# Kernel optimization log

Hardware: AMD Instinct MI355X
Metric: run time of the kernel (lower is better)

Reference implementation:

```python
import jax, jax.numpy as jnp
import numpy as np
from jax import lax

N_QUANTIZE = 256
N_AUX = 28
N_RESCH = 512
N_SKIPCH = 256
KS = 2
DILATIONS = [2 ** i for i in range(10)] * 3  # 30 layers
L = len(DILATIONS)


def _causal_conv(x, w, b, d):
    # x: (B, Cin, T), w: (Cout, Cin, KS) torch Conv1d layout, left-pad => causal
    pad = (w.shape[-1] - 1) * d
    y = lax.conv_general_dilated(x, w, window_strides=(1,), padding=[(pad, 0)],
                                 rhs_dilation=(d,),
                                 dimension_numbers=('NCH', 'OIH', 'NCH'))
    return y + b[None, :, None]


def _conv1x1(x, w, b):
    # x: (B, Cin, T), w: (Cout, Cin)
    return jnp.einsum('oi,bit->bot', w, x) + b[None, :, None]


def setup_inputs() -> dict:
    key = jax.random.key(0)
    ks = jax.random.split(key, 20)
    B, T = 2, 8000
    s = 0.05
    rn = lambda k, shape: (jax.random.normal(k, shape, jnp.float32) * s)
    inp = {
        'x': jax.random.randint(ks[0], (B, T), 0, N_QUANTIZE),
        'h': jax.random.normal(ks[1], (B, N_AUX, T), jnp.float32),
        'causal_w': rn(ks[2], (N_RESCH, N_QUANTIZE, KS)),
        'causal_b': rn(ks[3], (N_RESCH,)),
        'dil_sig_w': rn(ks[4], (L, N_RESCH, N_RESCH, KS)),
        'dil_sig_b': rn(ks[5], (L, N_RESCH)),
        'dil_tanh_w': rn(ks[6], (L, N_RESCH, N_RESCH, KS)),
        'dil_tanh_b': rn(ks[7], (L, N_RESCH)),
        'aux_sig_w': rn(ks[8], (L, N_RESCH, N_AUX)),
        'aux_sig_b': rn(ks[9], (L, N_RESCH)),
        'aux_tanh_w': rn(ks[10], (L, N_RESCH, N_AUX)),
        'aux_tanh_b': rn(ks[11], (L, N_RESCH)),
        'skip_w': rn(ks[12], (L, N_SKIPCH, N_RESCH)),
        'skip_b': rn(ks[13], (L, N_SKIPCH)),
        'res_w': rn(ks[14], (L, N_RESCH, N_RESCH)),
        'res_b': rn(ks[15], (L, N_RESCH)),
        'post1_w': rn(ks[16], (N_SKIPCH, N_SKIPCH)),
        'post1_b': rn(ks[17], (N_SKIPCH,)),
        'post2_w': rn(ks[18], (N_QUANTIZE, N_SKIPCH)),
        'post2_b': rn(ks[19], (N_QUANTIZE,)),
    }
    return inp


def reference(x, h, causal_w, causal_b, dil_sig_w, dil_sig_b, dil_tanh_w, dil_tanh_b,
              aux_sig_w, aux_sig_b, aux_tanh_w, aux_tanh_b, skip_w, skip_b,
              res_w, res_b, post1_w, post1_b, post2_w, post2_b):
    B, T = x.shape
    # _preprocess: onehot (B,T,Q) -> (B,Q,T), then causal conv
    oh = jax.nn.one_hot(x % N_QUANTIZE, N_QUANTIZE, dtype=jnp.float32).transpose(0, 2, 1)
    out = _causal_conv(oh, causal_w, causal_b, 1)  # (B, n_resch, T)
    skip_sum = jnp.zeros((B, N_SKIPCH, T), jnp.float32)
    for l, d in enumerate(DILATIONS):
        sig = _causal_conv(out, dil_sig_w[l], dil_sig_b[l], d) + _conv1x1(h, aux_sig_w[l], aux_sig_b[l])
        tan = _causal_conv(out, dil_tanh_w[l], dil_tanh_b[l], d) + _conv1x1(h, aux_tanh_w[l], aux_tanh_b[l])
        z = jax.nn.sigmoid(sig) * jnp.tanh(tan)
        skip_sum = skip_sum + _conv1x1(z, skip_w[l], skip_b[l])
        out = _conv1x1(z, res_w[l], res_b[l]) + out
    # _postprocess: relu -> 1x1 -> relu -> 1x1 -> (B, T, n_quantize)
    y = jax.nn.relu(skip_sum)
    y = jax.nn.relu(_conv1x1(y, post1_w, post1_b))
    y = _conv1x1(y, post2_w, post2_b)
    return y.transpose(0, 2, 1)
```

## Files before the change

### kernel.cpp

```cpp
#include <hip/hip_runtime.h>
#include <math.h>

#define T_LEN 8000
#define BATCH 2
#define CCH 512
#define SKP 256
#define AUXP 32
#define NQ 256
#define NLAYER 30
#define PADF 512
#define TPAD 8192
#define ROWS (PADF + TPAD)
#define HROWS TPAD

typedef unsigned short hfu;
typedef unsigned int u32;
typedef __attribute__((ext_vector_type(8))) _Float16 half8;
typedef __attribute__((ext_vector_type(4))) float f32x4;

#define GLOAD16(g, l)                                                          \
  __builtin_amdgcn_global_load_lds(                                            \
      (const __attribute__((address_space(1))) void*)(g),                      \
      (__attribute__((address_space(3))) void*)(l), 16, 0, 0)

__device__ inline hfu hfbits(float f) {
  union { _Float16 h; hfu u; } x;
  x.h = (_Float16)f;
  return x.u;
}
__device__ inline u32 pk2(float a, float b) {
  return (u32)hfbits(a) | ((u32)hfbits(b) << 16);
}
__device__ inline uint4 pk8(const float f[8]) {
  return make_uint4(pk2(f[0], f[1]), pk2(f[2], f[3]), pk2(f[4], f[5]), pk2(f[6], f[7]));
}
__device__ inline int ldsL(int row, int ck) {
  return ((row >> 1) << 3) + ((((ck) ^ ((row >> 1) & 3)) << 1) | (row & 1));
}

__global__ __launch_bounds__(256) void zero16(uint4* p, int n) {
  for (int i = blockIdx.x * 256 + threadIdx.x; i < n; i += gridDim.x * 256)
    p[i] = make_uint4(0u, 0u, 0u, 0u);
}

__global__ __launch_bounds__(256) void cvt_dil2(const float* __restrict__ inS,
                                                const float* __restrict__ inT,
                                                hfu* __restrict__ outS, hfu* __restrict__ outT) {
  const long NG = (long)NLAYER * CCH * (CCH / 4);
  for (long g2 = (long)blockIdx.x * 256 + threadIdx.x; g2 < 2 * NG; g2 += (long)gridDim.x * 256) {
    const int sel = (int)(g2 >= NG);
    const long g = sel ? (g2 - NG) : g2;
    const float* in = sel ? inT : inS;
    hfu* out = sel ? outT : outS;
    const int i4 = (int)(g & 127) * 4;
    const int o = (int)((g >> 7) & 511);
    const int l = (int)(g >> 16);
    const float* pp = in + (((size_t)l * CCH + o) * CCH + i4) * 2;
    float4 f0 = *(const float4*)pp;
    float4 f1 = *(const float4*)(pp + 4);
    uint2 t0 = make_uint2(pk2(f0.x, f0.z), pk2(f1.x, f1.z));
    uint2 t1 = make_uint2(pk2(f0.y, f0.w), pk2(f1.y, f1.w));
    hfu* ob = out + ((size_t)l * 2 * CCH + o) * CCH + i4;
    *(uint2*)ob = t0;
    *(uint2*)(ob + (size_t)CCH * CCH) = t1;
  }
}

__global__ __launch_bounds__(256) void cvt_skipres(const float* __restrict__ skw,
                                                   const float* __restrict__ rsw,
                                                   hfu* __restrict__ out) {
  const long NG = (long)NLAYER * 768 * (CCH / 4);
  for (long g = (long)blockIdx.x * 256 + threadIdx.x; g < NG; g += (long)gridDim.x * 256) {
    const int i4 = (int)(g & 127) * 4;
    const int r = (int)((g >> 7) % 768);
    const int l = (int)(g / (128 * 768));
    const float* src = (r < SKP) ? (skw + ((size_t)l * SKP + r) * CCH + i4)
                                 : (rsw + ((size_t)l * CCH + (r - SKP)) * CCH + i4);
    float4 f = *(const float4*)src;
    *(uint2*)(out + ((size_t)l * 768 + r) * CCH + i4) = make_uint2(pk2(f.x, f.y), pk2(f.z, f.w));
  }
}

__global__ __launch_bounds__(256) void cvt_aux(const float* __restrict__ in, hfu* __restrict__ out) {
  const int N = NLAYER * CCH * AUXP;
  for (int i = blockIdx.x * 256 + threadIdx.x; i < N; i += gridDim.x * 256) {
    const int j = i & 31;
    const int o = (i >> 5) & 511;
    const int l = i >> 14;
    float v = (j < 28) ? in[((size_t)l * CCH + o) * 28 + j] : 0.f;
    out[i] = hfbits(v);
  }
}

__global__ __launch_bounds__(256) void cvt_copy(const float* __restrict__ in, hfu* __restrict__ out, int n) {
  for (int i = blockIdx.x * 256 + threadIdx.x; i < n; i += gridDim.x * 256)
    out[i] = hfbits(in[i]);
}

__global__ __launch_bounds__(256) void cvt_cwt(const float* __restrict__ cw, float* __restrict__ out) {
  const int N = 2 * NQ * CCH;
  for (int i = blockIdx.x * 256 + threadIdx.x; i < N; i += gridDim.x * 256) {
    const int tap = i >> 17;
    const int r = i & 131071;
    const int xq = r >> 9;
    const int o = r & 511;
    out[i] = cw[((size_t)o * NQ + xq) * 2 + tap];
  }
}

__global__ __launch_bounds__(256) void htrans_kernel(const float* __restrict__ h, hfu* __restrict__ hbf) {
  const int b = blockIdx.y;
  const int t = blockIdx.x * 64 + (threadIdx.x & 63);
  const int j0 = threadIdx.x >> 6;
#pragma unroll
  for (int j = j0; j < AUXP; j += 4) {
    float v = (j < 28 && t < T_LEN) ? h[((size_t)b * 28 + j) * T_LEN + t] : 0.f;
    hbf[((size_t)b * HROWS + t) * AUXP + j] = hfbits(v);
  }
}

template <int PRE>
__global__ __launch_bounds__(256) void embed_kernel(const int* __restrict__ x,
                                                    const float* __restrict__ cwt,
                                                    const float* __restrict__ cb,
                                                    float* __restrict__ outf,
                                                    hfu* __restrict__ outb) {
  const int b = blockIdx.y;
  const int t = blockIdx.x * 4 + (threadIdx.x >> 6);
  const int o = (threadIdx.x & 63) * 8;
  const int xc = x[(size_t)b * T_LEN + t] & 255;
  const int xp = (t > 0) ? (x[(size_t)b * T_LEN + t - 1] & 255) : 0;
  const float won = (t > 0) ? 1.f : 0.f;
  const float* c1 = cwt + 131072 + (size_t)xc * CCH + o;
  const float* c0 = cwt + (size_t)xp * CCH + o;
  float v[8];
#pragma unroll
  for (int j = 0; j < 8; ++j) v[j] = cb[o + j] + c1[j] + won * c0[j];
  if (PRE) {
    *(uint4*)&outb[((size_t)b * ROWS + PADF + t) * CCH + o] = pk8(v);
  } else {
    float* po = outf + ((size_t)b * ROWS + PADF + t) * CCH + o;
    *(float4*)po = make_float4(v[0], v[1], v[2], v[3]);
    *(float4*)(po + 4) = make_float4(v[4], v[5], v[6], v[7]);
  }
}

template <int PRE>
__global__ __launch_bounds__(512, 2) void gate_kernel(
    const hfu* __restrict__ actb, const float* __restrict__ actf,
    const hfu* __restrict__ hbf,
    const void* __restrict__ wsp, const void* __restrict__ wtp,
    const hfu* __restrict__ auxs, const hfu* __restrict__ auxt,
    const float* __restrict__ bs1, const float* __restrict__ bs2,
    const float* __restrict__ bt1, const float* __restrict__ bt2,
    hfu* __restrict__ z, int d) {
  extern __shared__ uint4 smd[];
  const int tid = threadIdx.x;
  const int lane = tid & 63, wid = tid >> 6;
  const int wm = wid >> 2, wn = wid & 3;
  const int lr = lane & 15, lq = lane >> 4;

  const int n = blockIdx.x;
  const int f = (n & 7) * 32 + (n >> 3);
  const int tt = f >> 3, inner = f & 7;
  const int o0 = (inner >> 1) * 128;
  const int b = inner & 1;
  const int t0 = tt * 256;

  f32x4 accS[4][4] = {};
  f32x4 accT[4][4] = {};

  auto stage_dil = [&](int ih, int p) {
    const int base = p * 4096;
    const int tau = (ih < 8) ? 1 : 0;
    const int koff = (ih & 7) * 64;
    if (PRE) {
#pragma unroll
      for (int c = 0; c < 2; ++c) {
        const int s = c * 512 + tid;
        const int row = s >> 3, ck = (s & 7) ^ (row & 7);
        const size_t wo = ((size_t)tau * CCH + o0 + row) * CCH + koff + ck * 8;
        GLOAD16((const hfu*)wsp + wo, &smd[base + s]);
        GLOAD16((const hfu*)wtp + wo, &smd[base + 1024 + s]);
      }
#pragma unroll
      for (int c = 0; c < 4; ++c) {
        const int s = c * 512 + tid;
        const int row = s >> 3, ck = (s & 7) ^ (row & 7);
        const hfu* ar = actb + ((size_t)b * ROWS + PADF + t0 + row - (tau ? 0 : d)) * CCH + koff + ck * 8;
        GLOAD16(ar, &smd[base + 2048 + s]);
      }
    } else {
      const float* wsf = (const float*)wsp;
      const float* wtf = (const float*)wtp;
#pragma unroll
      for (int c = 0; c < 2; ++c) {
        const int s = c * 512 + tid;
        const int row = s >> 3, ck = (s & 7) ^ (row & 7);
        const size_t fb = ((size_t)(o0 + row) * CCH + koff + ck * 8) * 2;
        float vs[8], vt[8];
#pragma unroll
        for (int j = 0; j < 4; ++j) {
          float4 fs = *(const float4*)&wsf[fb + j * 4];
          float4 ft = *(const float4*)&wtf[fb + j * 4];
          vs[2 * j] = tau ? fs.y : fs.x;
          vs[2 * j + 1] = tau ? fs.w : fs.z;
          vt[2 * j] = tau ? ft.y : ft.x;
          vt[2 * j + 1] = tau ? ft.w : ft.z;
        }
        smd[base + s] = pk8(vs);
        smd[base + 1024 + s] = pk8(vt);
      }
#pragma unroll
      for (int c = 0; c < 4; ++c) {
        const int s = c * 512 + tid;
        const int row = s >> 3, ck = (s & 7) ^ (row & 7);
        const float* ar = actf + ((size_t)b * ROWS + PADF + t0 + row - (tau ? 0 : d)) * CCH + koff + ck * 8;
        float4 f0 = *(const float4*)&ar[0];
        float4 f1 = *(const float4*)&ar[4];
        float vb[8] = {f0.x, f0.y, f0.z, f0.w, f1.x, f1.y, f1.z, f1.w};
        smd[base + 2048 + s] = pk8(vb);
      }
    }
  };

  auto stage_aux = [&](int p) {
    const int base = p * 4096;
    {
      const int row = tid >> 2, ck = (tid & 3) ^ (row & 3);
      if (PRE) {
        GLOAD16(auxs + (size_t)(o0 + row) * AUXP + ck * 8, &smd[base + tid]);
        GLOAD16(auxt + (size_t)(o0 + row) * AUXP + ck * 8, &smd[base + 1024 + tid]);
      } else {
        smd[base + tid] = *(const uint4*)&auxs[(size_t)(o0 + row) * AUXP + ck * 8];
        smd[base + 1024 + tid] = *(const uint4*)&auxt[(size_t)(o0 + row) * AUXP + ck * 8];
      }
    }
#pragma unroll
    for (int c = 0; c < 2; ++c) {
      const int s = c * 512 + tid;
      const int row = s >> 2, ck = (s & 3) ^ (row & 3);
      if (PRE)
        GLOAD16(hbf + ((size_t)b * HROWS + t0 + row) * AUXP + ck * 8, &smd[base + 2048 + s]);
      else
        smd[base + 2048 + s] = *(const uint4*)&hbf[((size_t)b * HROWS + t0 + row) * AUXP + ck * 8];
    }
  };

  auto compute_dil = [&](int p) {
    const int base = p * 4096;
#pragma unroll
    for (int kk = 0; kk < 2; ++kk) {
      half8 af[4], ag[4], bv[4];
#pragma unroll
      for (int mr = 0; mr < 4; ++mr) {
        const int row = wm * 64 + mr * 16 + lr;
        const int idx = row * 8 + ((kk * 4 + lq) ^ (row & 7));
        af[mr] = *(const half8*)&smd[base + idx];
        ag[mr] = *(const half8*)&smd[base + 1024 + idx];
      }
#pragma unroll
      for (int nr = 0; nr < 4; ++nr) {
        const int row = wn * 64 + nr * 16 + lr;
        bv[nr] = *(const half8*)&smd[base + 2048 + row * 8 + ((kk * 4 + lq) ^ (row & 7))];
      }
#pragma unroll
      for (int mr = 0; mr < 4; ++mr)
#pragma unroll
        for (int nr = 0; nr < 4; ++nr) {
          accS[mr][nr] = __builtin_amdgcn_mfma_f32_16x16x32_f16(af[mr], bv[nr], accS[mr][nr], 0, 0, 0);
          accT[mr][nr] = __builtin_amdgcn_mfma_f32_16x16x32_f16(ag[mr], bv[nr], accT[mr][nr], 0, 0, 0);
        }
    }
  };

  auto compute_aux = [&](int p) {
    const int base = p * 4096;
    half8 af[4], ag[4], bv[4];
#pragma unroll
    for (int mr = 0; mr < 4; ++mr) {
      const int row = wm * 64 + mr * 16 + lr;
      const int idx = row * 4 + (lq ^ (row & 3));
      af[mr] = *(const half8*)&smd[base + idx];
      ag[mr] = *(const half8*)&smd[base + 1024 + idx];
    }
#pragma unroll
    for (int nr = 0; nr < 4; ++nr) {
      const int row = wn * 64 + nr * 16 + lr;
      bv[nr] = *(const half8*)&smd[base + 2048 + row * 4 + (lq ^ (row & 3))];
    }
#pragma unroll
    for (int mr = 0; mr < 4; ++mr)
#pragma unroll
      for (int nr = 0; nr < 4; ++nr) {
        accS[mr][nr] = __builtin_amdgcn_mfma_f32_16x16x32_f16(af[mr], bv[nr], accS[mr][nr], 0, 0, 0);
        accT[mr][nr] = __builtin_amdgcn_mfma_f32_16x16x32_f16(ag[mr], bv[nr], accT[mr][nr], 0, 0, 0);
      }
  };

  if (PRE) {
    stage_dil(0, 0);
    for (int ih = 0; ih < 17; ++ih) {
      if (ih < 15) {
        stage_dil(ih + 1, (ih + 1) & 1);
        asm volatile("s_waitcnt vmcnt(8)" ::: "memory");
      } else if (ih == 15) {
        stage_aux(0);
        asm volatile("s_waitcnt vmcnt(4)" ::: "memory");
      } else {
        asm volatile("s_waitcnt vmcnt(0)" ::: "memory");
      }
      __builtin_amdgcn_s_barrier();
      __builtin_amdgcn_sched_barrier(0);
      __builtin_amdgcn_s_setprio(1);
      if (ih < 16) compute_dil(ih & 1); else compute_aux(0);
      __builtin_amdgcn_s_setprio(0);
      __builtin_amdgcn_sched_barrier(0);
      __builtin_amdgcn_s_barrier();
    }
  } else {
    for (int ih = 0; ih < 17; ++ih) {
      if (ih < 16) stage_dil(ih, ih & 1); else stage_aux(0);
      __syncthreads();
      if (ih < 16) compute_dil(ih & 1); else compute_aux(0);
      __syncthreads();
    }
  }

#pragma unroll
  for (int mr = 0; mr < 4; ++mr) {
    const int ob = o0 + wm * 64 + mr * 16 + lq * 4;
    float4 x1 = *(const float4*)&bs1[ob];
    float4 x2 = *(const float4*)&bs2[ob];
    float4 y1 = *(const float4*)&bt1[ob];
    float4 y2 = *(const float4*)&bt2[ob];
    const float sb[4] = {x1.x + x2.x, x1.y + x2.y, x1.z + x2.z, x1.w + x2.w};
    const float tb[4] = {y1.x + y2.x, y1.y + y2.y, y1.z + y2.z, y1.w + y2.w};
#pragma unroll
    for (int nr = 0; nr < 4; ++nr) {
      const int t = t0 + wn * 64 + nr * 16 + lr;
      float zv[4];
#pragma unroll
      for (int j = 0; j < 4; ++j) {
        float sv = accS[mr][nr][j] + sb[j];
        float tv = accT[mr][nr][j] + tb[j];
        float sg = __builtin_amdgcn_rcpf(1.f + __expf(-sv));
        float e2 = __expf(2.f * tv);
        float th = 1.f - 2.f * __builtin_amdgcn_rcpf(e2 + 1.f);
        zv[j] = sg * th;
      }
      *(uint2*)&z[((size_t)b * HROWS + t) * CCH + ob] = make_uint2(pk2(zv[0], zv[1]), pk2(zv[2], zv[3]));
    }
  }
}

template <int PRE>
__global__ __launch_bounds__(512, 4) void update_kernel(
    const hfu* __restrict__ z, const void* __restrict__ wp,
    const float* __restrict__ skwf, const float* __restrict__ rswf,
    const float* __restrict__ skb, const float* __restrict__ rsb,
    float* __restrict__ skip, hfu* __restrict__ skiph,
    float* __restrict__ outf, hfu* __restrict__ outb) {
  __shared__ uint4 sm[2048];
  const int tid = threadIdx.x;
  const int lane = tid & 63, wid = tid >> 6;
  const int wm = wid >> 1, wn = wid & 1;
  const int lr = lane & 15, lq = lane >> 4;

  const int n = blockIdx.x;
  const int xcd = n & 7, j = n >> 3;
  const int ttl = j / 12, inner = j % 12;
  const int tt = xcd * 8 + ttl;
  if (tt > 62) return;
  const int rg = inner >> 1, b = inner & 1;
  const int r0 = rg * 128;
  const int t0 = tt * 128;

  f32x4 acc[2][4] = {};

  auto stage_u = [&](int ih, int p) {
    const int base = p * 1024;
    const int pr = tid >> 3, w = tid & 7;
    const int row = (pr << 1) | (w & 1);
    const int ck = (w >> 1) ^ (pr & 3);
    const int k0 = ih * 32;
    if (PRE) {
      GLOAD16((const hfu*)wp + (size_t)(r0 + row) * CCH + k0 + ck * 8, &sm[base + tid]);
      GLOAD16(z + ((size_t)b * HROWS + t0 + row) * CCH + k0 + ck * 8, &sm[base + 512 + tid]);
    } else {
      const int R = r0 + row;
      const float* src = (R < SKP) ? (skwf + (size_t)R * CCH + k0 + ck * 8)
                                   : (rswf + (size_t)(R - SKP) * CCH + k0 + ck * 8);
      float4 f0 = *(const float4*)&src[0];
      float4 f1 = *(const float4*)&src[4];
      float v[8] = {f0.x, f0.y, f0.z, f0.w, f1.x, f1.y, f1.z, f1.w};
      sm[base + tid] = pk8(v);
      sm[base + 512 + tid] = *(const uint4*)&z[((size_t)b * HROWS + t0 + row) * CCH + k0 + ck * 8];
    }
  };

  auto compute_u = [&](int p) {
    const int base = p * 1024;
    half8 av[2], bv[4];
#pragma unroll
    for (int mr = 0; mr < 2; ++mr) {
      const int row = wm * 32 + mr * 16 + lr;
      av[mr] = *(const half8*)&sm[base + ldsL(row, lq)];
    }
#pragma unroll
    for (int nr = 0; nr < 4; ++nr) {
      const int row = wn * 64 + nr * 16 + lr;
      bv[nr] = *(const half8*)&sm[base + 512 + ldsL(row, lq)];
    }
#pragma unroll
    for (int mr = 0; mr < 2; ++mr)
#pragma unroll
      for (int nr = 0; nr < 4; ++nr)
        acc[mr][nr] = __builtin_amdgcn_mfma_f32_16x16x32_f16(av[mr], bv[nr], acc[mr][nr], 0, 0, 0);
  };

  if (PRE) {
    stage_u(0, 0);
    for (int ih = 0; ih < 16; ++ih) {
      if (ih < 15) {
        stage_u(ih + 1, (ih + 1) & 1);
        asm volatile("s_waitcnt vmcnt(2)" ::: "memory");
      } else {
        asm volatile("s_waitcnt vmcnt(0)" ::: "memory");
      }
      __builtin_amdgcn_s_barrier();
      __builtin_amdgcn_sched_barrier(0);
      __builtin_amdgcn_s_setprio(1);
      compute_u(ih & 1);
      __builtin_amdgcn_s_setprio(0);
      __builtin_amdgcn_sched_barrier(0);
      __builtin_amdgcn_s_barrier();
    }
  } else {
    for (int ih = 0; ih < 16; ++ih) {
      stage_u(ih, ih & 1);
      __syncthreads();
      compute_u(ih & 1);
      __syncthreads();
    }
  }

  const bool iskip = (r0 < SKP);
#pragma unroll
  for (int mr = 0; mr < 2; ++mr) {
    const int R = r0 + wm * 32 + mr * 16 + lq * 4;
#pragma unroll
    for (int nr = 0; nr < 4; ++nr) {
      const int t = t0 + wn * 64 + nr * 16 + lr;
      if (t < T_LEN) {
        if (iskip) {
          float4 bb = *(const float4*)&skb[R];
          if (PRE) {
            hfu* ps = &skiph[((size_t)b * T_LEN + t) * SKP + R];
            uint2 old = *(uint2*)ps;
            const _Float16* hp = (const _Float16*)&old;
            float v0 = (float)hp[0] + acc[mr][nr][0] + bb.x;
            float v1 = (float)hp[1] + acc[mr][nr][1] + bb.y;
            float v2 = (float)hp[2] + acc[mr][nr][2] + bb.z;
            float v3 = (float)hp[3] + acc[mr][nr][3] + bb.w;
            *(uint2*)ps = make_uint2(pk2(v0, v1), pk2(v2, v3));
          } else {
            float4* p = (float4*)&skip[((size_t)b * T_LEN + t) * SKP + R];
            float4 v = *p;
            v.x += acc[mr][nr][0] + bb.x;
            v.y += acc[mr][nr][1] + bb.y;
            v.z += acc[mr][nr][2] + bb.z;
            v.w += acc[mr][nr][3] + bb.w;
            *p = v;
          }
        } else {
          const int rr = R - SKP;
          float4 bb = *(const float4*)&rsb[rr];
          if (PRE) {
            hfu* pb = &outb[((size_t)b * ROWS + PADF + t) * CCH + rr];
            uint2 old = *(uint2*)pb;
            const _Float16* hp = (const _Float16*)&old;
            float v0 = (float)hp[0] + acc[mr][nr][0] + bb.x;
            float v1 = (float)hp[1] + acc[mr][nr][1] + bb.y;
            float v2 = (float)hp[2] + acc[mr][nr][2] + bb.z;
            float v3 = (float)hp[3] + acc[mr][nr][3] + bb.w;
            *(uint2*)pb = make_uint2(pk2(v0, v1), pk2(v2, v3));
          } else {
            float4* p = (float4*)&outf[((size_t)b * ROWS + PADF + t) * CCH + rr];
            float4 v = *p;
            v.x += acc[mr][nr][0] + bb.x;
            v.y += acc[mr][nr][1] + bb.y;
            v.z += acc[mr][nr][2] + bb.z;
            v.w += acc[mr][nr][3] + bb.w;
            *p = v;
          }
        }
      }
    }
  }
}

template <int PRE>
__global__ __launch_bounds__(256, 2) void post1_kernel(const float* __restrict__ skip,
                                                       const hfu* __restrict__ skiph,
                                                       const hfu* __restrict__ w,
                                                       const float* __restrict__ bias,
                                                       hfu* __restrict__ y1) {
  __shared__ uint4 sm[2048];
  uint4* sA = sm;
  uint4* sB = sm + 1024;
  const int tid = threadIdx.x;
  const int lane = tid & 63, wid = tid >> 6;
  const int wm = wid >> 1, wn = wid & 1;
  const int lr = lane & 15, lq = lane >> 4;
  const int t0 = blockIdx.x * 128;
  const int r0 = blockIdx.y * 128;
  const int b = blockIdx.z;
  f32x4 acc[4][4] = {};
  for (int kt = 0; kt < 4; ++kt) {
#pragma unroll
    for (int c = 0; c < 4; ++c) {
      const int cb = c * 256 + wid * 64;
      const int ch = cb + lane;
      const int ksub = ch >> 7, mn = ch & 127;
      const int k0 = kt * 64 + ksub * 8;
      GLOAD16(w + (size_t)(r0 + mn) * SKP + k0, &sA[cb]);
      int row = t0 + mn;
      if (row > T_LEN - 1) row = T_LEN - 1;
      if (PRE) {
        uint4 u = *(const uint4*)&skiph[((size_t)b * T_LEN + row) * SKP + k0];
        const _Float16* hp = (const _Float16*)&u;
        float v[8];
#pragma unroll
        for (int j = 0; j < 8; ++j) v[j] = fmaxf((float)hp[j], 0.f);
        sB[ch] = pk8(v);
      } else {
        const float* src = skip + ((size_t)b * T_LEN + row) * SKP + k0;
        float4 f0 = *(const float4*)&src[0];
        float4 f1 = *(const float4*)&src[4];
        float v[8] = {fmaxf(f0.x, 0.f), fmaxf(f0.y, 0.f), fmaxf(f0.z, 0.f), fmaxf(f0.w, 0.f),
                      fmaxf(f1.x, 0.f), fmaxf(f1.y, 0.f), fmaxf(f1.z, 0.f), fmaxf(f1.w, 0.f)};
        sB[ch] = pk8(v);
      }
    }
    __syncthreads();
#pragma unroll
    for (int ks = 0; ks < 2; ++ks) {
      const int kb = (ks * 4 + lq) * 128;
      half8 av[4], bv[4];
#pragma unroll
      for (int r = 0; r < 4; ++r) {
        av[r] = *(const half8*)&sA[kb + wm * 64 + r * 16 + lr];
        bv[r] = *(const half8*)&sB[kb + wn * 64 + r * 16 + lr];
      }
#pragma unroll
      for (int mr = 0; mr < 4; ++mr)
#pragma unroll
        for (int nr = 0; nr < 4; ++nr)
          acc[mr][nr] = __builtin_amdgcn_mfma_f32_16x16x32_f16(av[mr], bv[nr], acc[mr][nr], 0, 0, 0);
    }
    __syncthreads();
  }
#pragma unroll
  for (int mr = 0; mr < 4; ++mr) {
    const int ob = r0 + wm * 64 + mr * 16 + lq * 4;
    float4 bb = *(const float4*)&bias[ob];
    const float bs[4] = {bb.x, bb.y, bb.z, bb.w};
#pragma unroll
    for (int nr = 0; nr < 4; ++nr) {
      const int t = t0 + wn * 64 + nr * 16 + lr;
      float v[4];
#pragma unroll
      for (int j = 0; j < 4; ++j) v[j] = fmaxf(acc[mr][nr][j] + bs[j], 0.f);
      *(uint2*)&y1[((size_t)b * HROWS + t) * SKP + ob] = make_uint2(pk2(v[0], v[1]), pk2(v[2], v[3]));
    }
  }
}

__global__ __launch_bounds__(256, 2) void post2_kernel(const hfu* __restrict__ y1,
                                                       const hfu* __restrict__ w,
                                                       const float* __restrict__ bias,
                                                       float* __restrict__ outp) {
  __shared__ uint4 sm[2048];
  uint4* sA = sm;
  uint4* sB = sm + 1024;
  const int tid = threadIdx.x;
  const int lane = tid & 63, wid = tid >> 6;
  const int wm = wid >> 1, wn = wid & 1;
  const int lr = lane & 15, lq = lane >> 4;
  const int t0 = blockIdx.x * 128;
  const int r0 = blockIdx.y * 128;
  const int b = blockIdx.z;
  f32x4 acc[4][4] = {};
  for (int kt = 0; kt < 4; ++kt) {
#pragma unroll
    for (int c = 0; c < 4; ++c) {
      const int cb = c * 256 + wid * 64;
      const int ch = cb + lane;
      const int ksub = ch >> 7, mn = ch & 127;
      const int k0 = kt * 64 + ksub * 8;
      GLOAD16(w + (size_t)(r0 + mn) * SKP + k0, &sA[cb]);
      GLOAD16(y1 + ((size_t)b * HROWS + t0 + mn) * SKP + k0, &sB[cb]);
    }
    __syncthreads();
#pragma unroll
    for (int ks = 0; ks < 2; ++ks) {
      const int kb = (ks * 4 + lq) * 128;
      half8 av[4], bv[4];
#pragma unroll
      for (int r = 0; r < 4; ++r) {
        av[r] = *(const half8*)&sA[kb + wm * 64 + r * 16 + lr];
        bv[r] = *(const half8*)&sB[kb + wn * 64 + r * 16 + lr];
      }
#pragma unroll
      for (int mr = 0; mr < 4; ++mr)
#pragma unroll
        for (int nr = 0; nr < 4; ++nr)
          acc[mr][nr] = __builtin_amdgcn_mfma_f32_16x16x32_f16(av[mr], bv[nr], acc[mr][nr], 0, 0, 0);
    }
    __syncthreads();
  }
#pragma unroll
  for (int mr = 0; mr < 4; ++mr) {
    const int ob = r0 + wm * 64 + mr * 16 + lq * 4;
    float4 bb = *(const float4*)&bias[ob];
#pragma unroll
    for (int nr = 0; nr < 4; ++nr) {
      const int t = t0 + wn * 64 + nr * 16 + lr;
      if (t < T_LEN) {
        float4 v;
        v.x = acc[mr][nr][0] + bb.x;
        v.y = acc[mr][nr][1] + bb.y;
        v.z = acc[mr][nr][2] + bb.z;
        v.w = acc[mr][nr][3] + bb.w;
        *(float4*)&outp[((size_t)b * T_LEN + t) * NQ + ob] = v;
      }
    }
  }
}

extern "C" void kernel_launch(void* const* d_in, const int* in_sizes, int n_in,
                              void* d_out, int out_size, void* d_ws, size_t ws_size,
                              hipStream_t stream) {
  const int* x = (const int*)d_in[0];
  const float* h = (const float*)d_in[1];
  const float* causal_w = (const float*)d_in[2];
  const float* causal_b = (const float*)d_in[3];
  const float* dil_sig_w = (const float*)d_in[4];
  const float* dil_sig_b = (const float*)d_in[5];
  const float* dil_tanh_w = (const float*)d_in[6];
  const float* dil_tanh_b = (const float*)d_in[7];
  const float* aux_sig_w = (const float*)d_in[8];
  const float* aux_sig_b = (const float*)d_in[9];
  const float* aux_tanh_w = (const float*)d_in[10];
  const float* aux_tanh_b = (const float*)d_in[11];
  const float* skip_w = (const float*)d_in[12];
  const float* skip_b = (const float*)d_in[13];
  const float* res_w = (const float*)d_in[14];
  const float* res_b = (const float*)d_in[15];
  const float* post1_w = (const float*)d_in[16];
  const float* post1_b = (const float*)d_in[17];
  const float* post2_w = (const float*)d_in[18];
  const float* post2_b = (const float*)d_in[19];
  float* outp = (float*)d_out;

  hipFuncSetAttribute((const void*)gate_kernel<1>,
                      hipFuncAttributeMaxDynamicSharedMemorySize, 131072);
  hipFuncSetAttribute((const void*)gate_kernel<0>,
                      hipFuncAttributeMaxDynamicSharedMemorySize, 131072);

  char* p = (char*)d_ws;
  auto alloc = [&](size_t bytes) {
    char* r = p;
    p += (bytes + 255) & ~(size_t)255;
    return r;
  };
  float* outf = (float*)alloc((size_t)BATCH * ROWS * CCH * 4);
  float* skip = (float*)alloc((size_t)BATCH * T_LEN * SKP * 4);
  hfu* zb = (hfu*)alloc((size_t)BATCH * HROWS * CCH * 2);
  hfu* hbf = (hfu*)alloc((size_t)BATCH * HROWS * AUXP * 2);
  hfu* auxsb = (hfu*)alloc((size_t)NLAYER * CCH * AUXP * 2);
  hfu* auxtb = (hfu*)alloc((size_t)NLAYER * CCH * AUXP * 2);
  hfu* p1b = (hfu*)alloc((size_t)NQ * SKP * 2);
  hfu* p2b = (hfu*)alloc((size_t)NQ * SKP * 2);
  float* cwt = (float*)alloc((size_t)2 * NQ * CCH * 4);
  hfu* skiph = (hfu*)alloc((size_t)BATCH * T_LEN * SKP * 2);
  hfu* y1 = zb;
  hfu* outb = (hfu*)alloc((size_t)BATCH * ROWS * CCH * 2);
  hfu* dilS = (hfu*)alloc((size_t)NLAYER * 2 * CCH * CCH * 2);
  hfu* dilT = (hfu*)alloc((size_t)NLAYER * 2 * CCH * CCH * 2);
  hfu* wsr = (hfu*)alloc((size_t)NLAYER * 768 * CCH * 2);
  const bool pre = ((size_t)(p - (char*)d_ws) <= ws_size);

  cvt_aux<<<256, 256, 0, stream>>>(aux_sig_w, auxsb);
  cvt_aux<<<256, 256, 0, stream>>>(aux_tanh_w, auxtb);
  cvt_copy<<<64, 256, 0, stream>>>(post1_w, p1b, NQ * SKP);
  cvt_copy<<<64, 256, 0, stream>>>(post2_w, p2b, NQ * SKP);
  cvt_cwt<<<1024, 256, 0, stream>>>(causal_w, cwt);
  if (pre) {
    cvt_dil2<<<4096, 256, 0, stream>>>(dil_sig_w, dil_tanh_w, dilS, dilT);
    cvt_skipres<<<2048, 256, 0, stream>>>(skip_w, res_w, wsr);
  }

  if (pre) {
    zero16<<<512, 256, 0, stream>>>((uint4*)skiph, (int)((size_t)BATCH * T_LEN * SKP * 2 / 16));
    for (int b = 0; b < BATCH; ++b) {
      zero16<<<32, 256, 0, stream>>>((uint4*)(outb + (size_t)b * ROWS * CCH), PADF * CCH * 2 / 16);
      zero16<<<48, 256, 0, stream>>>((uint4*)(outb + ((size_t)b * ROWS + PADF + T_LEN) * CCH),
                                     (TPAD - T_LEN) * CCH * 2 / 16);
    }
  } else {
    zero16<<<512, 256, 0, stream>>>((uint4*)skip, (int)((size_t)BATCH * T_LEN * SKP * 4 / 16));
    for (int b = 0; b < BATCH; ++b) {
      zero16<<<64, 256, 0, stream>>>((uint4*)(outf + (size_t)b * ROWS * CCH), PADF * CCH * 4 / 16);
      zero16<<<96, 256, 0, stream>>>((uint4*)(outf + ((size_t)b * ROWS + PADF + T_LEN) * CCH),
                                     (TPAD - T_LEN) * CCH * 4 / 16);
    }
  }

  htrans_kernel<<<dim3(128, 2), 256, 0, stream>>>(h, hbf);
  if (pre)
    embed_kernel<1><<<dim3(2000, 2), 256, 0, stream>>>(x, cwt, causal_b, nullptr, outb);
  else
    embed_kernel<0><<<dim3(2000, 2), 256, 0, stream>>>(x, cwt, causal_b, outf, nullptr);

  for (int l = 0; l < NLAYER; ++l) {
    const int d = 1 << (l % 10);
    if (pre) {
      gate_kernel<1><<<256, 512, 131072, stream>>>(
          outb, nullptr, hbf, dilS + (size_t)l * 2 * CCH * CCH, dilT + (size_t)l * 2 * CCH * CCH,
          auxsb + (size_t)l * CCH * AUXP, auxtb + (size_t)l * CCH * AUXP,
          dil_sig_b + (size_t)l * CCH, aux_sig_b + (size_t)l * CCH,
          dil_tanh_b + (size_t)l * CCH, aux_tanh_b + (size_t)l * CCH, zb, d);
      update_kernel<1><<<768, 512, 0, stream>>>(
          zb, wsr + (size_t)l * 768 * CCH, nullptr, nullptr,
          skip_b + (size_t)l * SKP, res_b + (size_t)l * CCH, nullptr, skiph, nullptr, outb);
    } else {
      gate_kernel<0><<<256, 512, 131072, stream>>>(
          nullptr, outf, hbf, dil_sig_w + (size_t)l * CCH * CCH * 2,
          dil_tanh_w + (size_t)l * CCH * CCH * 2,
          auxsb + (size_t)l * CCH * AUXP, auxtb + (size_t)l * CCH * AUXP,
          dil_sig_b + (size_t)l * CCH, aux_sig_b + (size_t)l * CCH,
          dil_tanh_b + (size_t)l * CCH, aux_tanh_b + (size_t)l * CCH, zb, d);
      update_kernel<0><<<768, 512, 0, stream>>>(
          zb, nullptr, skip_w + (size_t)l * SKP * CCH, res_w + (size_t)l * CCH * CCH,
          skip_b + (size_t)l * SKP, res_b + (size_t)l * CCH, skip, nullptr, outf, nullptr);
    }
  }

  if (pre)
    post1_kernel<1><<<dim3(63, 2, BATCH), 256, 0, stream>>>(nullptr, skiph, p1b, post1_b, y1);
  else
    post1_kernel<0><<<dim3(63, 2, BATCH), 256, 0, stream>>>(skip, nullptr, p1b, post1_b, y1);
  post2_kernel<<<dim3(63, 2, BATCH), 256, 0, stream>>>(y1, p2b, post2_b, outp);
}
```

Before: 2.087 ms.

## Triple-buffer gate and update GEMM pipelines with K=32 stages and pointer increments

The gate and update kernels move from double-buffered K=64 stages to triple-buffered K=32 stages, issuing loads three stages ahead and waiting on vmcnt counts. Global addresses are advanced by pointer increments instead of being recomputed, and the LDS read offsets are precomputed once. The gate kernel's dynamic LDS drops from 131072 to 98304 bytes, which could allow higher occupancy. The dilated-weight conversion is widened to 8 elements per thread, and the finer stage granularity adds more barriers per K sweep.

```diff
diff --git a/kernel.cpp b/kernel.cpp
--- a/kernel.cpp
+++ b/kernel.cpp
@@ -43,26 +43,28 @@
     p[i] = make_uint4(0u, 0u, 0u, 0u);
 }
 
-__global__ __launch_bounds__(256) void cvt_dil2(const float* __restrict__ inS,
-                                                const float* __restrict__ inT,
-                                                hfu* __restrict__ outS, hfu* __restrict__ outT) {
-  const long NG = (long)NLAYER * CCH * (CCH / 4);
+__global__ __launch_bounds__(256) void cvt_dil2b(const float* __restrict__ inS,
+                                                 const float* __restrict__ inT,
+                                                 hfu* __restrict__ outS, hfu* __restrict__ outT) {
+  const long NG = (long)NLAYER * CCH * (CCH / 8);
   for (long g2 = (long)blockIdx.x * 256 + threadIdx.x; g2 < 2 * NG; g2 += (long)gridDim.x * 256) {
     const int sel = (int)(g2 >= NG);
     const long g = sel ? (g2 - NG) : g2;
     const float* in = sel ? inT : inS;
     hfu* out = sel ? outT : outS;
-    const int i4 = (int)(g & 127) * 4;
-    const int o = (int)((g >> 7) & 511);
-    const int l = (int)(g >> 16);
-    const float* pp = in + (((size_t)l * CCH + o) * CCH + i4) * 2;
-    float4 f0 = *(const float4*)pp;
-    float4 f1 = *(const float4*)(pp + 4);
-    uint2 t0 = make_uint2(pk2(f0.x, f0.z), pk2(f1.x, f1.z));
-    uint2 t1 = make_uint2(pk2(f0.y, f0.w), pk2(f1.y, f1.w));
-    hfu* ob = out + ((size_t)l * 2 * CCH + o) * CCH + i4;
-    *(uint2*)ob = t0;
-    *(uint2*)(ob + (size_t)CCH * CCH) = t1;
+    const int i8 = (int)(g & 63) * 8;
+    const int o = (int)((g >> 6) & 511);
+    const int l = (int)(g >> 15);
+    const float* pp = in + (((size_t)l * CCH + o) * CCH + i8) * 2;
+    float4 a = *(const float4*)pp;
+    float4 bq = *(const float4*)(pp + 4);
+    float4 c = *(const float4*)(pp + 8);
+    float4 e = *(const float4*)(pp + 12);
+    const float t0[8] = {a.x, a.z, bq.x, bq.z, c.x, c.z, e.x, e.z};
+    const float t1[8] = {a.y, a.w, bq.y, bq.w, c.y, c.w, e.y, e.w};
+    hfu* ob = out + ((size_t)l * 2 * CCH + o) * CCH + i8;
+    *(uint4*)ob = pk8(t0);
+    *(uint4*)(ob + (size_t)CCH * CCH) = pk8(t1);
   }
 }
 
@@ -167,36 +169,86 @@
   const int b = inner & 1;
   const int t0 = tt * 256;
 
+  const int row = 2 * (tid >> 3) + (tid & 1);
+  const int ck = ((tid & 7) >> 1) ^ ((tid >> 3) & 3);
+
   f32x4 accS[4][4] = {};
   f32x4 accT[4][4] = {};
 
-  auto stage_dil = [&](int ih, int p) {
-    const int base = p * 4096;
-    const int tau = (ih < 8) ? 1 : 0;
-    const int koff = (ih & 7) * 64;
-    if (PRE) {
-#pragma unroll
-      for (int c = 0; c < 2; ++c) {
-        const int s = c * 512 + tid;
-        const int row = s >> 3, ck = (s & 7) ^ (row & 7);
-        const size_t wo = ((size_t)tau * CCH + o0 + row) * CCH + koff + ck * 8;
-        GLOAD16((const hfu*)wsp + wo, &smd[base + s]);
-        GLOAD16((const hfu*)wtp + wo, &smd[base + 1024 + s]);
-      }
-#pragma unroll
-      for (int c = 0; c < 4; ++c) {
-        const int s = c * 512 + tid;
-        const int row = s >> 3, ck = (s & 7) ^ (row & 7);
-        const hfu* ar = actb + ((size_t)b * ROWS + PADF + t0 + row - (tau ? 0 : d)) * CCH + koff + ck * 8;
-        GLOAD16(ar, &smd[base + 2048 + s]);
-      }
-    } else {
-      const float* wsf = (const float*)wsp;
-      const float* wtf = (const float*)wtp;
-#pragma unroll
-      for (int c = 0; c < 2; ++c) {
-        const int s = c * 512 + tid;
-        const int row = s >> 3, ck = (s & 7) ^ (row & 7);
+  if (PRE) {
+    const hfu* wsPtr = (const hfu*)wsp + ((size_t)CCH + o0 + row) * CCH + ck * 8;
+    const hfu* wtPtr = (const hfu*)wtp + ((size_t)CCH + o0 + row) * CCH + ck * 8;
+    const hfu* bP0 = actb + ((size_t)b * ROWS + PADF + t0 + row) * CCH + ck * 8;
+    const hfu* bP1 = bP0 + (size_t)128 * CCH;
+    int offA[4], offB[4];
+#pragma unroll
+    for (int mr = 0; mr < 4; ++mr) offA[mr] = ldsL(wm * 64 + mr * 16 + lr, lq);
+#pragma unroll
+    for (int nr = 0; nr < 4; ++nr) offB[nr] = ldsL(wn * 64 + nr * 16 + lr, lq);
+
+    auto stage = [&](int ihs) {
+      uint4* dst = smd + (ihs % 3) * 2048;
+      if (ihs < 32) {
+        GLOAD16(wsPtr, &dst[tid]);
+        GLOAD16(wtPtr, &dst[512 + tid]);
+        GLOAD16(bP0, &dst[1024 + tid]);
+        GLOAD16(bP1, &dst[1536 + tid]);
+        if (ihs == 15) {
+          wsPtr -= (size_t)CCH * CCH + 480;
+          wtPtr -= (size_t)CCH * CCH + 480;
+          bP0 -= 480 + (size_t)d * CCH;
+          bP1 -= 480 + (size_t)d * CCH;
+        } else {
+          wsPtr += 32; wtPtr += 32; bP0 += 32; bP1 += 32;
+        }
+      } else {
+        GLOAD16(auxs + (size_t)(o0 + row) * AUXP + ck * 8, &dst[tid]);
+        GLOAD16(auxt + (size_t)(o0 + row) * AUXP + ck * 8, &dst[512 + tid]);
+        GLOAD16(hbf + ((size_t)b * HROWS + t0 + row) * AUXP + ck * 8, &dst[1024 + tid]);
+        GLOAD16(hbf + ((size_t)b * HROWS + t0 + 128 + row) * AUXP + ck * 8, &dst[1536 + tid]);
+      }
+    };
+
+    stage(0); stage(1); stage(2);
+    for (int ih = 0; ih < 33; ++ih) {
+      if (ih <= 30)
+        asm volatile("s_waitcnt vmcnt(8)" ::: "memory");
+      else if (ih == 31)
+        asm volatile("s_waitcnt vmcnt(4)" ::: "memory");
+      else
+        asm volatile("s_waitcnt vmcnt(0)" ::: "memory");
+      __builtin_amdgcn_s_barrier();
+      __builtin_amdgcn_sched_barrier(0);
+      const uint4* base = smd + (ih % 3) * 2048;
+      half8 af[4], ag[4], bv[4];
+#pragma unroll
+      for (int mr = 0; mr < 4; ++mr) {
+        af[mr] = *(const half8*)&base[offA[mr]];
+        ag[mr] = *(const half8*)&base[512 + offA[mr]];
+      }
+#pragma unroll
+      for (int nr = 0; nr < 4; ++nr) bv[nr] = *(const half8*)&base[1024 + offB[nr]];
+      __builtin_amdgcn_s_setprio(1);
+#pragma unroll
+      for (int mr = 0; mr < 4; ++mr)
+#pragma unroll
+        for (int nr = 0; nr < 4; ++nr) {
+          accS[mr][nr] = __builtin_amdgcn_mfma_f32_16x16x32_f16(af[mr], bv[nr], accS[mr][nr], 0, 0, 0);
+          accT[mr][nr] = __builtin_amdgcn_mfma_f32_16x16x32_f16(ag[mr], bv[nr], accT[mr][nr], 0, 0, 0);
+        }
+      __builtin_amdgcn_s_setprio(0);
+      __builtin_amdgcn_sched_barrier(0);
+      __builtin_amdgcn_s_barrier();
+      if (ih <= 29) stage(ih + 3);
+    }
+  } else {
+    for (int ih = 0; ih < 33; ++ih) {
+      uint4* dst = smd + (ih % 3) * 2048;
+      if (ih < 32) {
+        const int tau = (ih < 16) ? 1 : 0;
+        const int koff = (ih & 15) * 32;
+        const float* wsf = (const float*)wsp;
+        const float* wtf = (const float*)wtp;
         const size_t fb = ((size_t)(o0 + row) * CCH + koff + ck * 8) * 2;
         float vs[8], vt[8];
 #pragma unroll
@@ -208,62 +260,35 @@
           vt[2 * j] = tau ? ft.y : ft.x;
           vt[2 * j + 1] = tau ? ft.w : ft.z;
         }
-        smd[base + s] = pk8(vs);
-        smd[base + 1024 + s] = pk8(vt);
-      }
-#pragma unroll
-      for (int c = 0; c < 4; ++c) {
-        const int s = c * 512 + tid;
-        const int row = s >> 3, ck = (s & 7) ^ (row & 7);
-        const float* ar = actf + ((size_t)b * ROWS + PADF + t0 + row - (tau ? 0 : d)) * CCH + koff + ck * 8;
-        float4 f0 = *(const float4*)&ar[0];
-        float4 f1 = *(const float4*)&ar[4];
-        float vb[8] = {f0.x, f0.y, f0.z, f0.w, f1.x, f1.y, f1.z, f1.w};
-        smd[base + 2048 + s] = pk8(vb);
-      }
-    }
-  };
-
-  auto stage_aux = [&](int p) {
-    const int base = p * 4096;
-    {
-      const int row = tid >> 2, ck = (tid & 3) ^ (row & 3);
-      if (PRE) {
-        GLOAD16(auxs + (size_t)(o0 + row) * AUXP + ck * 8, &smd[base + tid]);
-        GLOAD16(auxt + (size_t)(o0 + row) * AUXP + ck * 8, &smd[base + 1024 + tid]);
+        dst[tid] = pk8(vs);
+        dst[512 + tid] = pk8(vt);
+#pragma unroll
+        for (int c = 0; c < 2; ++c) {
+          const int rr = row + c * 128;
+          const float* ar = actf + ((size_t)b * ROWS + PADF + t0 + rr - (tau ? 0 : d)) * CCH + koff + ck * 8;
+          float4 f0 = *(const float4*)&ar[0];
+          float4 f1 = *(const float4*)&ar[4];
+          float vb[8] = {f0.x, f0.y, f0.z, f0.w, f1.x, f1.y, f1.z, f1.w};
+          dst[1024 + c * 512 + tid] = pk8(vb);
+        }
       } else {
-        smd[base + tid] = *(const uint4*)&auxs[(size_t)(o0 + row) * AUXP + ck * 8];
-        smd[base + 1024 + tid] = *(const uint4*)&auxt[(size_t)(o0 + row) * AUXP + ck * 8];
-      }
-    }
-#pragma unroll
-    for (int c = 0; c < 2; ++c) {
-      const int s = c * 512 + tid;
-      const int row = s >> 2, ck = (s & 3) ^ (row & 3);
-      if (PRE)
-        GLOAD16(hbf + ((size_t)b * HROWS + t0 + row) * AUXP + ck * 8, &smd[base + 2048 + s]);
-      else
-        smd[base + 2048 + s] = *(const uint4*)&hbf[((size_t)b * HROWS + t0 + row) * AUXP + ck * 8];
-    }
-  };
-
-  auto compute_dil = [&](int p) {
-    const int base = p * 4096;
-#pragma unroll
-    for (int kk = 0; kk < 2; ++kk) {
+        dst[tid] = *(const uint4*)&auxs[(size_t)(o0 + row) * AUXP + ck * 8];
+        dst[512 + tid] = *(const uint4*)&auxt[(size_t)(o0 + row) * AUXP + ck * 8];
+        dst[1024 + tid] = *(const uint4*)&hbf[((size_t)b * HROWS + t0 + row) * AUXP + ck * 8];
+        dst[1536 + tid] = *(const uint4*)&hbf[((size_t)b * HROWS + t0 + 128 + row) * AUXP + ck * 8];
+      }
+      __syncthreads();
+      const uint4* base = smd + (ih % 3) * 2048;
       half8 af[4], ag[4], bv[4];
 #pragma unroll
       for (int mr = 0; mr < 4; ++mr) {
-        const int row = wm * 64 + mr * 16 + lr;
-        const int idx = row * 8 + ((kk * 4 + lq) ^ (row & 7));
-        af[mr] = *(const half8*)&smd[base + idx];
-        ag[mr] = *(const half8*)&smd[base + 1024 + idx];
-      }
-#pragma unroll
-      for (int nr = 0; nr < 4; ++nr) {
-        const int row = wn * 64 + nr * 16 + lr;
-        bv[nr] = *(const half8*)&smd[base + 2048 + row * 8 + ((kk * 4 + lq) ^ (row & 7))];
-      }
+        const int idx = ldsL(wm * 64 + mr * 16 + lr, lq);
+        af[mr] = *(const half8*)&base[idx];
+        ag[mr] = *(const half8*)&base[512 + idx];
+      }
+#pragma unroll
+      for (int nr = 0; nr < 4; ++nr)
+        bv[nr] = *(const half8*)&base[1024 + ldsL(wn * 64 + nr * 16 + lr, lq)];
 #pragma unroll
       for (int mr = 0; mr < 4; ++mr)
 #pragma unroll
@@ -271,58 +296,6 @@
           accS[mr][nr] = __builtin_amdgcn_mfma_f32_16x16x32_f16(af[mr], bv[nr], accS[mr][nr], 0, 0, 0);
           accT[mr][nr] = __builtin_amdgcn_mfma_f32_16x16x32_f16(ag[mr], bv[nr], accT[mr][nr], 0, 0, 0);
         }
-    }
-  };
-
-  auto compute_aux = [&](int p) {
-    const int base = p * 4096;
-    half8 af[4], ag[4], bv[4];
-#pragma unroll
-    for (int mr = 0; mr < 4; ++mr) {
-      const int row = wm * 64 + mr * 16 + lr;
-      const int idx = row * 4 + (lq ^ (row & 3));
-      af[mr] = *(const half8*)&smd[base + idx];
-      ag[mr] = *(const half8*)&smd[base + 1024 + idx];
-    }
-#pragma unroll
-    for (int nr = 0; nr < 4; ++nr) {
-      const int row = wn * 64 + nr * 16 + lr;
-      bv[nr] = *(const half8*)&smd[base + 2048 + row * 4 + (lq ^ (row & 3))];
-    }
-#pragma unroll
-    for (int mr = 0; mr < 4; ++mr)
-#pragma unroll
-      for (int nr = 0; nr < 4; ++nr) {
-        accS[mr][nr] = __builtin_amdgcn_mfma_f32_16x16x32_f16(af[mr], bv[nr], accS[mr][nr], 0, 0, 0);
-        accT[mr][nr] = __builtin_amdgcn_mfma_f32_16x16x32_f16(ag[mr], bv[nr], accT[mr][nr], 0, 0, 0);
-      }
-  };
-
-  if (PRE) {
-    stage_dil(0, 0);
-    for (int ih = 0; ih < 17; ++ih) {
-      if (ih < 15) {
-        stage_dil(ih + 1, (ih + 1) & 1);
-        asm volatile("s_waitcnt vmcnt(8)" ::: "memory");
-      } else if (ih == 15) {
-        stage_aux(0);
-        asm volatile("s_waitcnt vmcnt(4)" ::: "memory");
-      } else {
-        asm volatile("s_waitcnt vmcnt(0)" ::: "memory");
-      }
-      __builtin_amdgcn_s_barrier();
-      __builtin_amdgcn_sched_barrier(0);
-      __builtin_amdgcn_s_setprio(1);
-      if (ih < 16) compute_dil(ih & 1); else compute_aux(0);
-      __builtin_amdgcn_s_setprio(0);
-      __builtin_amdgcn_sched_barrier(0);
-      __builtin_amdgcn_s_barrier();
-    }
-  } else {
-    for (int ih = 0; ih < 17; ++ih) {
-      if (ih < 16) stage_dil(ih, ih & 1); else stage_aux(0);
-      __syncthreads();
-      if (ih < 16) compute_dil(ih & 1); else compute_aux(0);
       __syncthreads();
     }
   }
@@ -361,7 +334,7 @@
     const float* __restrict__ skb, const float* __restrict__ rsb,
     float* __restrict__ skip, hfu* __restrict__ skiph,
     float* __restrict__ outf, hfu* __restrict__ outb) {
-  __shared__ uint4 sm[2048];
+  __shared__ uint4 sm[3072];
   const int tid = threadIdx.x;
   const int lane = tid & 63, wid = tid >> 6;
   const int wm = wid >> 1, wn = wid & 1;
@@ -377,70 +350,75 @@
   const int t0 = tt * 128;
 
   f32x4 acc[2][4] = {};
-
-  auto stage_u = [&](int ih, int p) {
-    const int base = p * 1024;
-    const int pr = tid >> 3, w = tid & 7;
-    const int row = (pr << 1) | (w & 1);
-    const int ck = (w >> 1) ^ (pr & 3);
-    const int k0 = ih * 32;
-    if (PRE) {
-      GLOAD16((const hfu*)wp + (size_t)(r0 + row) * CCH + k0 + ck * 8, &sm[base + tid]);
-      GLOAD16(z + ((size_t)b * HROWS + t0 + row) * CCH + k0 + ck * 8, &sm[base + 512 + tid]);
-    } else {
+  const int row = 2 * (tid >> 3) + (tid & 1);
+  const int ck = ((tid & 7) >> 1) ^ ((tid >> 3) & 3);
+
+  if (PRE) {
+    const hfu* wPtr = (const hfu*)wp + (size_t)(r0 + row) * CCH + ck * 8;
+    const hfu* zPtr = z + ((size_t)b * HROWS + t0 + row) * CCH + ck * 8;
+    int offa[2], offb[4];
+#pragma unroll
+    for (int mr = 0; mr < 2; ++mr) offa[mr] = ldsL(wm * 32 + mr * 16 + lr, lq);
+#pragma unroll
+    for (int nr = 0; nr < 4; ++nr) offb[nr] = ldsL(wn * 64 + nr * 16 + lr, lq);
+
+    auto stage_u = [&](int ihs) {
+      uint4* dst = sm + (ihs % 3) * 1024;
+      GLOAD16(wPtr, &dst[tid]);
+      GLOAD16(zPtr, &dst[512 + tid]);
+      wPtr += 32; zPtr += 32;
+    };
+    stage_u(0); stage_u(1); stage_u(2);
+    for (int ih = 0; ih < 16; ++ih) {
+      if (ih <= 13)
+        asm volatile("s_waitcnt vmcnt(4)" ::: "memory");
+      else if (ih == 14)
+        asm volatile("s_waitcnt vmcnt(2)" ::: "memory");
+      else
+        asm volatile("s_waitcnt vmcnt(0)" ::: "memory");
+      __builtin_amdgcn_s_barrier();
+      __builtin_amdgcn_sched_barrier(0);
+      const uint4* base = sm + (ih % 3) * 1024;
+      half8 av[2], bv[4];
+#pragma unroll
+      for (int mr = 0; mr < 2; ++mr) av[mr] = *(const half8*)&base[offa[mr]];
+#pragma unroll
+      for (int nr = 0; nr < 4; ++nr) bv[nr] = *(const half8*)&base[512 + offb[nr]];
+      __builtin_amdgcn_s_setprio(1);
+#pragma unroll
+      for (int mr = 0; mr < 2; ++mr)
+#pragma unroll
+        for (int nr = 0; nr < 4; ++nr)
+          acc[mr][nr] = __builtin_amdgcn_mfma_f32_16x16x32_f16(av[mr], bv[nr], acc[mr][nr], 0, 0, 0);
+      __builtin_amdgcn_s_setprio(0);
+      __builtin_amdgcn_sched_barrier(0);
+      __builtin_amdgcn_s_barrier();
+      if (ih <= 12) stage_u(ih + 3);
+    }
+  } else {
+    for (int ih = 0; ih < 16; ++ih) {
+      uint4* dst = sm + (ih % 3) * 1024;
+      const int k0 = ih * 32;
       const int R = r0 + row;
       const float* src = (R < SKP) ? (skwf + (size_t)R * CCH + k0 + ck * 8)
                                    : (rswf + (size_t)(R - SKP) * CCH + k0 + ck * 8);
       float4 f0 = *(const float4*)&src[0];
       float4 f1 = *(const float4*)&src[4];
       float v[8] = {f0.x, f0.y, f0.z, f0.w, f1.x, f1.y, f1.z, f1.w};
-      sm[base + tid] = pk8(v);
-      sm[base + 512 + tid] = *(const uint4*)&z[((size_t)b * HROWS + t0 + row) * CCH + k0 + ck * 8];
-    }
-  };
-
-  auto compute_u = [&](int p) {
-    const int base = p * 1024;
-    half8 av[2], bv[4];
-#pragma unroll
-    for (int mr = 0; mr < 2; ++mr) {
-      const int row = wm * 32 + mr * 16 + lr;
-      av[mr] = *(const half8*)&sm[base + ldsL(row, lq)];
-    }
-#pragma unroll
-    for (int nr = 0; nr < 4; ++nr) {
-      const int row = wn * 64 + nr * 16 + lr;
-      bv[nr] = *(const half8*)&sm[base + 512 + ldsL(row, lq)];
-    }
-#pragma unroll
-    for (int mr = 0; mr < 2; ++mr)
-#pragma unroll
-      for (int nr = 0; nr < 4; ++nr)
-        acc[mr][nr] = __builtin_amdgcn_mfma_f32_16x16x32_f16(av[mr], bv[nr], acc[mr][nr], 0, 0, 0);
-  };
-
-  if (PRE) {
-    stage_u(0, 0);
-    for (int ih = 0; ih < 16; ++ih) {
-      if (ih < 15) {
-        stage_u(ih + 1, (ih + 1) & 1);
-        asm volatile("s_waitcnt vmcnt(2)" ::: "memory");
-      } else {
-        asm volatile("s_waitcnt vmcnt(0)" ::: "memory");
-      }
-      __builtin_amdgcn_s_barrier();
-      __builtin_amdgcn_sched_barrier(0);
-      __builtin_amdgcn_s_setprio(1);
-      compute_u(ih & 1);
-      __builtin_amdgcn_s_setprio(0);
-      __builtin_amdgcn_sched_barrier(0);
-      __builtin_amdgcn_s_barrier();
-    }
-  } else {
-    for (int ih = 0; ih < 16; ++ih) {
-      stage_u(ih, ih & 1);
+      dst[tid] = pk8(v);
+      dst[512 + tid] = *(const uint4*)&z[((size_t)b * HROWS + t0 + row) * CCH + k0 + ck * 8];
       __syncthreads();
-      compute_u(ih & 1);
+      const uint4* base = sm + (ih % 3) * 1024;
+      half8 av[2], bv[4];
+#pragma unroll
+      for (int mr = 0; mr < 2; ++mr) av[mr] = *(const half8*)&base[ldsL(wm * 32 + mr * 16 + lr, lq)];
+#pragma unroll
+      for (int nr = 0; nr < 4; ++nr) bv[nr] = *(const half8*)&base[512 + ldsL(wn * 64 + nr * 16 + lr, lq)];
+#pragma unroll
+      for (int mr = 0; mr < 2; ++mr)
+#pragma unroll
+        for (int nr = 0; nr < 4; ++nr)
+          acc[mr][nr] = __builtin_amdgcn_mfma_f32_16x16x32_f16(av[mr], bv[nr], acc[mr][nr], 0, 0, 0);
       __syncthreads();
     }
   }
@@ -532,7 +510,7 @@
         const _Float16* hp = (const _Float16*)&u;
         float v[8];
 #pragma unroll
-        for (int j = 0; j < 8; ++j) v[j] = fmaxf((float)hp[j], 0.f);
+        for (int jj = 0; jj < 8; ++jj) v[jj] = fmaxf((float)hp[jj], 0.f);
         sB[ch] = pk8(v);
       } else {
         const float* src = skip + ((size_t)b * T_LEN + row) * SKP + k0;
@@ -571,7 +549,7 @@
       const int t = t0 + wn * 64 + nr * 16 + lr;
       float v[4];
 #pragma unroll
-      for (int j = 0; j < 4; ++j) v[j] = fmaxf(acc[mr][nr][j] + bs[j], 0.f);
+      for (int jj = 0; jj < 4; ++jj) v[jj] = fmaxf(acc[mr][nr][jj] + bs[jj], 0.f);
       *(uint2*)&y1[((size_t)b * HROWS + t) * SKP + ob] = make_uint2(pk2(v[0], v[1]), pk2(v[2], v[3]));
     }
   }
@@ -665,9 +643,9 @@
   float* outp = (float*)d_out;
 
   hipFuncSetAttribute((const void*)gate_kernel<1>,
-                      hipFuncAttributeMaxDynamicSharedMemorySize, 131072);
+                      hipFuncAttributeMaxDynamicSharedMemorySize, 98304);
   hipFuncSetAttribute((const void*)gate_kernel<0>,
-                      hipFuncAttributeMaxDynamicSharedMemorySize, 131072);
+                      hipFuncAttributeMaxDynamicSharedMemorySize, 98304);
 
   char* p = (char*)d_ws;
   auto alloc = [&](size_t bytes) {
@@ -698,7 +676,7 @@
   cvt_copy<<<64, 256, 0, stream>>>(post2_w, p2b, NQ * SKP);
   cvt_cwt<<<1024, 256, 0, stream>>>(causal_w, cwt);
   if (pre) {
-    cvt_dil2<<<4096, 256, 0, stream>>>(dil_sig_w, dil_tanh_w, dilS, dilT);
+    cvt_dil2b<<<2048, 256, 0, stream>>>(dil_sig_w, dil_tanh_w, dilS, dilT);
     cvt_skipres<<<2048, 256, 0, stream>>>(skip_w, res_w, wsr);
   }
 
@@ -727,7 +705,7 @@
   for (int l = 0; l < NLAYER; ++l) {
     const int d = 1 << (l % 10);
     if (pre) {
-      gate_kernel<1><<<256, 512, 131072, stream>>>(
+      gate_kernel<1><<<256, 512, 98304, stream>>>(
           outb, nullptr, hbf, dilS + (size_t)l * 2 * CCH * CCH, dilT + (size_t)l * 2 * CCH * CCH,
           auxsb + (size_t)l * CCH * AUXP, auxtb + (size_t)l * CCH * AUXP,
           dil_sig_b + (size_t)l * CCH, aux_sig_b + (size_t)l * CCH,
@@ -736,7 +714,7 @@
           zb, wsr + (size_t)l * 768 * CCH, nullptr, nullptr,
           skip_b + (size_t)l * SKP, res_b + (size_t)l * CCH, nullptr, skiph, nullptr, outb);
     } else {
-      gate_kernel<0><<<256, 512, 131072, stream>>>(
+      gate_kernel<0><<<256, 512, 98304, stream>>>(
           nullptr, outf, hbf, dil_sig_w + (size_t)l * CCH * CCH * 2,
           dil_tanh_w + (size_t)l * CCH * CCH * 2,
           auxsb + (size_t)l * CCH * AUXP, auxtb + (size_t)l * CCH * AUXP,
```

Result: slower. 2.165 ms (+3.7%).
